# Kernel tuning notes

Hardware: AMD Instinct MI355X
Metric: run time of the kernel (lower is better)

## Reference

```python
import jax, jax.numpy as jnp
import numpy as np

B, T, C, H = 4, 4096, 1024, 64  # batch, seq_len, n_embd, head_size


def setup_inputs() -> dict:
    key = jax.random.key(0)
    kx, kk, kq, kv = jax.random.split(key, 4)
    x = jax.random.normal(kx, (B, T, C), dtype=jnp.float32)
    Wk = jax.random.normal(kk, (C, H), dtype=jnp.float32) * (C ** -0.5)
    Wq = jax.random.normal(kq, (C, H), dtype=jnp.float32) * (C ** -0.5)
    Wv = jax.random.normal(kv, (C, H), dtype=jnp.float32) * (C ** -0.5)
    return {"x": x, "Wk": Wk, "Wq": Wq, "Wv": Wv}


def reference(x, Wk, Wq, Wv):
    # q,k,v: (B,T,H)
    k = jnp.einsum('btc,ch->bth', x, Wk)
    q = jnp.einsum('btc,ch->bth', x, Wq)
    v = jnp.einsum('btc,ch->bth', x, Wv)
    # NOTE: source scales by C**-0.5 (embedding dim), not head_size**-0.5
    scale = jnp.asarray(C, x.dtype) ** -0.5
    scores = jnp.einsum('bqh,bkh->bqk', q, k) * scale  # (B,T,T)
    causal = jnp.tril(jnp.ones((T, T), dtype=bool))
    scores = jnp.where(causal, scores, jnp.asarray(-jnp.inf, scores.dtype))
    weight = jax.nn.softmax(scores, axis=-1)
    out = jnp.einsum('bqk,bkh->bqh', weight, v)  # (B,T,H)
    return out
```

## Files before the change

### kernel.cpp

```cpp
#include <hip/hip_runtime.h>

typedef unsigned short u16;
typedef unsigned int u32;
typedef float v4f __attribute__((ext_vector_type(4)));
typedef __bf16 v8bf __attribute__((ext_vector_type(8)));

#define STR 72
#define VSTR 136

__device__ __forceinline__ u16 f2bf(float f) {
    union { float f; u32 u; } v; v.f = f;
    u32 r = v.u + 0x7fffu + ((v.u >> 16) & 1u);
    return (u16)(r >> 16);
}
__device__ __forceinline__ u32 pk2(float lo, float hi) {
    return ((u32)f2bf(hi) << 16) | (u32)f2bf(lo);
}
__device__ __forceinline__ u32 pk2t(float lo, float hi) {
    union { float f; u32 u; } a, b; a.f = hi; b.f = lo;
    return __builtin_amdgcn_perm(a.u, b.u, 0x07060302u);
}
__device__ __forceinline__ float bfLo(u32 p) {
    union { u32 u; float f; } v; v.u = p << 16; return v.f;
}
__device__ __forceinline__ float bfHi(u32 p) {
    union { u32 u; float f; } v; v.u = p & 0xffff0000u; return v.f;
}
__device__ __forceinline__ v4f zero4() { v4f z = {0.f, 0.f, 0.f, 0.f}; return z; }

__global__ __launch_bounds__(64) void prep_w(const float* __restrict__ Wk,
                                             const float* __restrict__ Wq,
                                             const float* __restrict__ Wv,
                                             u16* __restrict__ WtF) {
    const int f = blockIdx.x >> 5;
    const int ks = blockIdx.x & 31;
    const int lane = threadIdx.x;
    const int w = f >> 2;
    const float* W = (w == 0) ? Wk : ((w == 1) ? Wq : Wv);
    const int h = (f & 3) * 16 + (lane & 15);
    const int k0 = ks * 32 + (lane >> 4) * 8;
    u16 tmp[8];
#pragma unroll
    for (int j = 0; j < 8; ++j) tmp[j] = f2bf(W[(size_t)(k0 + j) * 64 + h]);
    *(uint4*)&WtF[((size_t)blockIdx.x * 64 + lane) * 8] = *(const uint4*)tmp;
}

__global__ __launch_bounds__(256, 4) void qkv_proj(const float* __restrict__ x,
                                                   const u16* __restrict__ WtF,
                                                   u16* __restrict__ kq,
                                                   u16* __restrict__ vT) {
    __shared__ v4f red[3][12][64];
    const int tid = threadIdx.x;
    const int lane = tid & 63;
    const int wv = tid >> 6;
    const int l15 = lane & 15, quad = lane >> 4;
    const int row0 = blockIdx.x * 16;

    v4f acc[12];
#pragma unroll
    for (int i = 0; i < 12; ++i) acc[i] = zero4();

    const float* xr = x + (size_t)(row0 + l15) * 1024 + wv * 256 + quad * 8;

    union { u32 u[4]; v8bf v; } af[8];
#pragma unroll
    for (int half = 0; half < 2; ++half) {
        float4 t[8];
#pragma unroll
        for (int i = 0; i < 8; ++i)
            t[i] = *(const float4*)(xr + half * 128 + (i >> 1) * 32 + (i & 1) * 4);
#pragma unroll
        for (int j = 0; j < 4; ++j) {
            int ks = half * 4 + j;
            af[ks].u[0] = pk2(t[2 * j].x, t[2 * j].y);
            af[ks].u[1] = pk2(t[2 * j].z, t[2 * j].w);
            af[ks].u[2] = pk2(t[2 * j + 1].x, t[2 * j + 1].y);
            af[ks].u[3] = pk2(t[2 * j + 1].z, t[2 * j + 1].w);
        }
    }

    const u16* wf0 = WtF + ((size_t)(wv * 8) * 64 + lane) * 8;
#pragma unroll
    for (int f = 0; f < 12; ++f) {
        const u16* wpf = wf0 + (size_t)f * 16384;
#pragma unroll
        for (int ks = 0; ks < 8; ++ks) {
            acc[f] = __builtin_amdgcn_mfma_f32_16x16x32_bf16(
                af[ks].v, *(const v8bf*)(wpf + ks * 512), acc[f], 0, 0, 0);
        }
    }

    if (wv > 0) {
#pragma unroll
        for (int f = 0; f < 12; ++f) red[wv - 1][f][lane] = acc[f];
    }
    __syncthreads();
    if (wv == 0) {
#pragma unroll
        for (int f = 0; f < 12; ++f) {
            acc[f] += red[0][f][lane];
            acc[f] += red[1][f][lane];
            acc[f] += red[2][f][lane];
        }
        const float QSC = 0.04508422002778f;
#pragma unroll
        for (int ct = 0; ct < 8; ++ct) {
            int w = ct >> 2, ht = ct & 3;
            float s = (w == 1) ? QSC : 1.f;
#pragma unroll
            for (int r = 0; r < 4; ++r)
                kq[((size_t)w * 16384 + row0 + quad * 4 + r) * 64 + ht * 16 + l15] =
                    f2bf(acc[ct][r] * s);
        }
        int tok = row0 + quad * 4;
        int b = tok >> 12, t = tok & 4095;
#pragma unroll
        for (int ct = 8; ct < 12; ++ct) {
            int h = (ct & 3) * 16 + l15;
            uint2 st = {pk2(acc[ct][0], acc[ct][1]), pk2(acc[ct][2], acc[ct][3])};
            *(uint2*)&vT[((size_t)(b * 64 + h)) * 4096 + t] = st;
        }
    }
}

__global__ __launch_bounds__(256) void attn_part(const u16* __restrict__ kq,
                                                 const u16* __restrict__ vT,
                                                 float* __restrict__ Op,
                                                 float* __restrict__ ml,
                                                 int KC, int MAXCH) {
    __shared__ u16 Kl[128][STR];
    __shared__ u16 Vl[64][VSTR];

    const int a = blockIdx.x, c = blockIdx.y, b = blockIdx.z;
    if (c * KC > a) return;

    const int tid  = threadIdx.x;
    const int lane = tid & 63;
    const int wv   = tid >> 6;
    const int l15  = lane & 15;
    const int quad = lane >> 4;
    const int queryg = a * 64 + wv * 16 + l15;

    const u16* kb = kq;
    const u16* qb = kq + (size_t)16384 * 64;

    v8bf qf0 = *(const v8bf*)&qb[((size_t)(b * 4096) + queryg) * 64 + quad * 8];
    v8bf qf1 = *(const v8bf*)&qb[((size_t)(b * 4096) + queryg) * 64 + 32 + quad * 8];

    v4f o[4];
#pragma unroll
    for (int i = 0; i < 4; ++i) o[i] = zero4();
    float suml = 0.f;

    const int kt0 = c * KC;
    const int kt1 = (kt0 + KC < a + 1) ? (kt0 + KC) : (a + 1);

    for (int kp = kt0; kp < kt1; kp += 2) {
        __syncthreads();
#pragma unroll
        for (int i = 0; i < 4; ++i) {
            int idx = tid + i * 256;
            int kr = idx >> 3, kc2 = (idx & 7) << 3;
            *(uint4*)&Kl[kr][kc2] =
                *(const uint4*)&kb[((size_t)(b * 4096 + kp * 64 + kr)) * 64 + kc2];
            int h = idx >> 4, kcol = (idx & 15) << 3;
            *(uint4*)&Vl[h][kcol] =
                *(const uint4*)&vT[((size_t)(b * 64 + h)) * 4096 + kp * 64 + kcol];
        }
        __syncthreads();

        const int nsub = (kp + 1 < kt1) ? 2 : 1;
        for (int h2 = 0; h2 < nsub; ++h2) {
            const int kt = kp + h2;

            v4f s[4];
#pragma unroll
            for (int ct = 0; ct < 4; ++ct) {
                v8bf ka0 = *(const v8bf*)&Kl[h2 * 64 + ct * 16 + l15][quad * 8];
                v8bf ka1 = *(const v8bf*)&Kl[h2 * 64 + ct * 16 + l15][32 + quad * 8];
                v4f t = zero4();
                t = __builtin_amdgcn_mfma_f32_16x16x32_bf16(ka0, qf0, t, 0, 0, 0);
                t = __builtin_amdgcn_mfma_f32_16x16x32_bf16(ka1, qf1, t, 0, 0, 0);
                s[ct] = t;
            }

            if (kt == a) {
                const int key0 = kt * 64 + quad * 4;
#pragma unroll
                for (int ct = 0; ct < 4; ++ct)
#pragma unroll
                    for (int r = 0; r < 4; ++r)
                        s[ct][r] = ((key0 + ct * 16 + r) > queryg) ? -1e30f : s[ct][r];
            }

            u32 pk[4][2];
#pragma unroll
            for (int ct = 0; ct < 4; ++ct) {
                float p0 = exp2f(s[ct][0]);
                float p1 = exp2f(s[ct][1]);
                float p2 = exp2f(s[ct][2]);
                float p3 = exp2f(s[ct][3]);
                u32 pa = pk2t(p0, p1), pb = pk2t(p2, p3);
                pk[ct][0] = pa; pk[ct][1] = pb;
                suml += (bfLo(pa) + bfHi(pa)) + (bfLo(pb) + bfHi(pb));
            }

            const int srcA = ((quad & 1) << 5) + l15;
            const int srcB = srcA + 16;
            const bool hi = (quad >= 2);
#pragma unroll
            for (int ks = 0; ks < 2; ++ks) {
                u32 g0a = (u32)__shfl((int)pk[ks * 2][0], srcA);
                u32 g0b = (u32)__shfl((int)pk[ks * 2 + 1][0], srcA);
                u32 g1a = (u32)__shfl((int)pk[ks * 2][1], srcA);
                u32 g1b = (u32)__shfl((int)pk[ks * 2 + 1][1], srcA);
                u32 g2a = (u32)__shfl((int)pk[ks * 2][0], srcB);
                u32 g2b = (u32)__shfl((int)pk[ks * 2 + 1][0], srcB);
                u32 g3a = (u32)__shfl((int)pk[ks * 2][1], srcB);
                u32 g3b = (u32)__shfl((int)pk[ks * 2 + 1][1], srcB);
                union { u32 u[4]; v8bf v; } pf;
                pf.u[0] = hi ? g0b : g0a;
                pf.u[1] = hi ? g1b : g1a;
                pf.u[2] = hi ? g2b : g2a;
                pf.u[3] = hi ? g3b : g3a;
#pragma unroll
                for (int ht = 0; ht < 4; ++ht) {
                    v8bf av = *(const v8bf*)&Vl[ht * 16 + l15][h2 * 64 + ks * 32 + quad * 8];
                    o[ht] = __builtin_amdgcn_mfma_f32_16x16x32_bf16(av, pf.v, o[ht], 0, 0, 0);
                }
            }
        }
    }

    suml += __shfl_xor(suml, 16);
    suml += __shfl_xor(suml, 32);

    size_t pidx = ((size_t)b * 64 + a) * MAXCH + c;
    float* op = Op + pidx * 4096;
#pragma unroll
    for (int ht = 0; ht < 4; ++ht)
#pragma unroll
        for (int r = 0; r < 4; ++r)
            op[(ht * 16 + quad * 4 + r) * 64 + wv * 16 + l15] = o[ht][r];
    if (quad == 0)
        ml[pidx * 64 + wv * 16 + l15] = suml;
}

__global__ __launch_bounds__(256) void attn_combine(const float* __restrict__ Op,
                                                    const float* __restrict__ ml,
                                                    float* __restrict__ out,
                                                    int KC, int MAXCH) {
    const int a = blockIdx.x, b = blockIdx.y;
    const int nch = a / KC + 1;
    const int tid = threadIdx.x;
    const int q = tid & 63, hq = tid >> 6;
    const size_t pbase = ((size_t)b * 64 + a) * MAXCH;

    float L = 0.f;
    float acc[16];
#pragma unroll
    for (int j = 0; j < 16; ++j) acc[j] = 0.f;
    for (int c = 0; c < nch; ++c) {
        L += ml[(pbase + c) * 64 + q];
        const float* op = Op + (pbase + c) * 4096;
#pragma unroll
        for (int j = 0; j < 16; ++j) acc[j] += op[(hq * 16 + j) * 64 + q];
    }
    float inv = 1.f / L;
    float* dst = &out[((size_t)b * 4096 + a * 64 + q) * 64 + hq * 16];
#pragma unroll
    for (int g = 0; g < 4; ++g) {
        float4 st = {acc[g * 4] * inv, acc[g * 4 + 1] * inv,
                     acc[g * 4 + 2] * inv, acc[g * 4 + 3] * inv};
        *(float4*)&dst[g * 4] = st;
    }
}

extern "C" void kernel_launch(void* const* d_in, const int* in_sizes, int n_in,
                              void* d_out, int out_size, void* d_ws, size_t ws_size,
                              hipStream_t stream) {
    const float* x  = (const float*)d_in[0];
    const float* Wk = (const float*)d_in[1];
    const float* Wq = (const float*)d_in[2];
    const float* Wv = (const float*)d_in[3];
    float* out = (float*)d_out;

    char* wsb = (char*)d_ws;
    u16* WtF = (u16*)wsb;
    u16* kq  = (u16*)(wsb + 393216);
    u16* vT  = (u16*)(wsb + 393216 + 4194304);
    const size_t base = 393216 + 4194304 + 2097152;

    int KC = 8, MAXCH = 8;
    while (KC < 64 && base + (size_t)256 * MAXCH * (4096 + 64) * 4 > ws_size) {
        KC <<= 1; MAXCH >>= 1;
    }
    float* Op = (float*)(wsb + base);
    float* ml = Op + (size_t)256 * MAXCH * 4096;

    prep_w<<<dim3(384), dim3(64), 0, stream>>>(Wk, Wq, Wv, WtF);
    qkv_proj<<<dim3(1024), dim3(256), 0, stream>>>(x, WtF, kq, vT);
    attn_part<<<dim3(64, MAXCH, 4), dim3(256), 0, stream>>>(kq, vT, Op, ml, KC, MAXCH);
    attn_combine<<<dim3(64, 4), dim3(256), 0, stream>>>(Op, ml, out, KC, MAXCH);
}
```

Baseline: 151.3 us.

## Load K and V fragments directly from global memory, dropping LDS staging

The attention kernel no longer stages K and V tiles in shared memory behind two barriers per tile pair. Each wave now loads its MFMA operand fragments straight from global memory (via L2/L1) one 64-key tile at a time. This removes the LDS write/read round trip and the __syncthreads calls. In exchange, all four waves fetch the same K/V data redundantly from cache and lose the two-tile batching.

```diff
diff --git a/kernel.cpp b/kernel.cpp
--- a/kernel.cpp
+++ b/kernel.cpp
@@ -4,9 +4,6 @@
 typedef unsigned int u32;
 typedef float v4f __attribute__((ext_vector_type(4)));
 typedef __bf16 v8bf __attribute__((ext_vector_type(8)));
-
-#define STR 72
-#define VSTR 136
 
 __device__ __forceinline__ u16 f2bf(float f) {
     union { float f; u32 u; } v; v.f = f;
@@ -128,9 +125,6 @@
                                                  float* __restrict__ Op,
                                                  float* __restrict__ ml,
                                                  int KC, int MAXCH) {
-    __shared__ u16 Kl[128][STR];
-    __shared__ u16 Vl[64][VSTR];
-
     const int a = blockIdx.x, c = blockIdx.y, b = blockIdx.z;
     if (c * KC > a) return;
 
@@ -155,79 +149,77 @@
     const int kt0 = c * KC;
     const int kt1 = (kt0 + KC < a + 1) ? (kt0 + KC) : (a + 1);
 
-    for (int kp = kt0; kp < kt1; kp += 2) {
-        __syncthreads();
-#pragma unroll
-        for (int i = 0; i < 4; ++i) {
-            int idx = tid + i * 256;
-            int kr = idx >> 3, kc2 = (idx & 7) << 3;
-            *(uint4*)&Kl[kr][kc2] =
-                *(const uint4*)&kb[((size_t)(b * 4096 + kp * 64 + kr)) * 64 + kc2];
-            int h = idx >> 4, kcol = (idx & 15) << 3;
-            *(uint4*)&Vl[h][kcol] =
-                *(const uint4*)&vT[((size_t)(b * 64 + h)) * 4096 + kp * 64 + kcol];
-        }
-        __syncthreads();
-
-        const int nsub = (kp + 1 < kt1) ? 2 : 1;
-        for (int h2 = 0; h2 < nsub; ++h2) {
-            const int kt = kp + h2;
-
-            v4f s[4];
-#pragma unroll
-            for (int ct = 0; ct < 4; ++ct) {
-                v8bf ka0 = *(const v8bf*)&Kl[h2 * 64 + ct * 16 + l15][quad * 8];
-                v8bf ka1 = *(const v8bf*)&Kl[h2 * 64 + ct * 16 + l15][32 + quad * 8];
-                v4f t = zero4();
-                t = __builtin_amdgcn_mfma_f32_16x16x32_bf16(ka0, qf0, t, 0, 0, 0);
-                t = __builtin_amdgcn_mfma_f32_16x16x32_bf16(ka1, qf1, t, 0, 0, 0);
-                s[ct] = t;
-            }
-
-            if (kt == a) {
-                const int key0 = kt * 64 + quad * 4;
-#pragma unroll
-                for (int ct = 0; ct < 4; ++ct)
-#pragma unroll
-                    for (int r = 0; r < 4; ++r)
-                        s[ct][r] = ((key0 + ct * 16 + r) > queryg) ? -1e30f : s[ct][r];
-            }
-
-            u32 pk[4][2];
-#pragma unroll
-            for (int ct = 0; ct < 4; ++ct) {
-                float p0 = exp2f(s[ct][0]);
-                float p1 = exp2f(s[ct][1]);
-                float p2 = exp2f(s[ct][2]);
-                float p3 = exp2f(s[ct][3]);
-                u32 pa = pk2t(p0, p1), pb = pk2t(p2, p3);
-                pk[ct][0] = pa; pk[ct][1] = pb;
-                suml += (bfLo(pa) + bfHi(pa)) + (bfLo(pb) + bfHi(pb));
-            }
-
-            const int srcA = ((quad & 1) << 5) + l15;
-            const int srcB = srcA + 16;
-            const bool hi = (quad >= 2);
-#pragma unroll
-            for (int ks = 0; ks < 2; ++ks) {
-                u32 g0a = (u32)__shfl((int)pk[ks * 2][0], srcA);
-                u32 g0b = (u32)__shfl((int)pk[ks * 2 + 1][0], srcA);
-                u32 g1a = (u32)__shfl((int)pk[ks * 2][1], srcA);
-                u32 g1b = (u32)__shfl((int)pk[ks * 2 + 1][1], srcA);
-                u32 g2a = (u32)__shfl((int)pk[ks * 2][0], srcB);
-                u32 g2b = (u32)__shfl((int)pk[ks * 2 + 1][0], srcB);
-                u32 g3a = (u32)__shfl((int)pk[ks * 2][1], srcB);
-                u32 g3b = (u32)__shfl((int)pk[ks * 2 + 1][1], srcB);
-                union { u32 u[4]; v8bf v; } pf;
-                pf.u[0] = hi ? g0b : g0a;
-                pf.u[1] = hi ? g1b : g1a;
-                pf.u[2] = hi ? g2b : g2a;
-                pf.u[3] = hi ? g3b : g3a;
-#pragma unroll
-                for (int ht = 0; ht < 4; ++ht) {
-                    v8bf av = *(const v8bf*)&Vl[ht * 16 + l15][h2 * 64 + ks * 32 + quad * 8];
-                    o[ht] = __builtin_amdgcn_mfma_f32_16x16x32_bf16(av, pf.v, o[ht], 0, 0, 0);
-                }
+    const u16* kfb = kb + ((size_t)(b * 4096 + l15) * 64) + quad * 8;
+    const u16* vfb = vT + ((size_t)(b * 64 + l15)) * 4096 + quad * 8;
+
+    for (int kt = kt0; kt < kt1; ++kt) {
+        v8bf ka[4][2];
+#pragma unroll
+        for (int ct = 0; ct < 4; ++ct) {
+            const u16* p = kfb + (size_t)(kt * 64 + ct * 16) * 64;
+            ka[ct][0] = *(const v8bf*)p;
+            ka[ct][1] = *(const v8bf*)(p + 32);
+        }
+        v8bf av[4][2];
+#pragma unroll
+        for (int ht = 0; ht < 4; ++ht) {
+            const u16* p = vfb + (size_t)(ht * 16) * 4096 + kt * 64;
+            av[ht][0] = *(const v8bf*)p;
+            av[ht][1] = *(const v8bf*)(p + 32);
+        }
+
+        v4f s[4];
+#pragma unroll
+        for (int ct = 0; ct < 4; ++ct) {
+            v4f t = zero4();
+            t = __builtin_amdgcn_mfma_f32_16x16x32_bf16(ka[ct][0], qf0, t, 0, 0, 0);
+            t = __builtin_amdgcn_mfma_f32_16x16x32_bf16(ka[ct][1], qf1, t, 0, 0, 0);
+            s[ct] = t;
+        }
+
+        if (kt == a) {
+            const int key0 = kt * 64 + quad * 4;
+#pragma unroll
+            for (int ct = 0; ct < 4; ++ct)
+#pragma unroll
+                for (int r = 0; r < 4; ++r)
+                    s[ct][r] = ((key0 + ct * 16 + r) > queryg) ? -1e30f : s[ct][r];
+        }
+
+        u32 pk[4][2];
+#pragma unroll
+        for (int ct = 0; ct < 4; ++ct) {
+            float p0 = exp2f(s[ct][0]);
+            float p1 = exp2f(s[ct][1]);
+            float p2 = exp2f(s[ct][2]);
+            float p3 = exp2f(s[ct][3]);
+            u32 pa = pk2t(p0, p1), pb = pk2t(p2, p3);
+            pk[ct][0] = pa; pk[ct][1] = pb;
+            suml += (bfLo(pa) + bfHi(pa)) + (bfLo(pb) + bfHi(pb));
+        }
+
+        const int srcA = ((quad & 1) << 5) + l15;
+        const int srcB = srcA + 16;
+        const bool hi = (quad >= 2);
+#pragma unroll
+        for (int ks = 0; ks < 2; ++ks) {
+            u32 g0a = (u32)__shfl((int)pk[ks * 2][0], srcA);
+            u32 g0b = (u32)__shfl((int)pk[ks * 2 + 1][0], srcA);
+            u32 g1a = (u32)__shfl((int)pk[ks * 2][1], srcA);
+            u32 g1b = (u32)__shfl((int)pk[ks * 2 + 1][1], srcA);
+            u32 g2a = (u32)__shfl((int)pk[ks * 2][0], srcB);
+            u32 g2b = (u32)__shfl((int)pk[ks * 2 + 1][0], srcB);
+            u32 g3a = (u32)__shfl((int)pk[ks * 2][1], srcB);
+            u32 g3b = (u32)__shfl((int)pk[ks * 2 + 1][1], srcB);
+            union { u32 u[4]; v8bf v; } pf;
+            pf.u[0] = hi ? g0b : g0a;
+            pf.u[1] = hi ? g1b : g1a;
+            pf.u[2] = hi ? g2b : g2a;
+            pf.u[3] = hi ? g3b : g3a;
+#pragma unroll
+            for (int ht = 0; ht < 4; ++ht) {
+                o[ht] = __builtin_amdgcn_mfma_f32_16x16x32_bf16(av[ht][ks], pf.v,
+                                                                o[ht], 0, 0, 0);
             }
         }
     }
```

Result: slower. 206.4 us (+36.4%).
